# Optimization experiments

Measured on AMD Instinct MI355X. Metric: run time of the kernel, lower is better.

The kernel has to match this reference:

```python
import jax, jax.numpy as jnp
import numpy as np

HID = 8
EMB = 32


def setup_inputs() -> dict:
    V = 32000
    S, B = 128, 32
    key = jax.random.key(0)
    ks = jax.random.split(key, 13)
    u = lambda k, shape, s: jax.random.uniform(k, shape, jnp.float32, -1.0 / np.sqrt(s), 1.0 / np.sqrt(s))
    return {
        "input_batch": jax.random.randint(ks[0], (S, B), 0, V, dtype=jnp.int64),
        "lookup": u(ks[1], (V, EMB), EMB),
        "weight_xf": u(ks[2], (EMB, HID), HID),
        "weight_hf": u(ks[3], (HID, HID), HID),
        "weight_xb": u(ks[4], (EMB, HID), HID),
        "weight_hb": u(ks[5], (HID, HID), HID),
        "weight_o": u(ks[6], (2 * HID, V), V),
        "Hf": u(ks[7], (HID,), HID),
        "Hb": u(ks[8], (HID,), HID),
        "bias_x": u(ks[9], (HID,), HID),
        "bias_hf": u(ks[10], (HID,), HID),
        "bias_hb": u(ks[11], (HID,), HID),
        "bias_o": u(ks[12], (V,), V),
    }


def reference(input_batch, lookup, weight_xf, weight_hf, weight_xb, weight_hb,
              weight_o, Hf, Hb, bias_x, bias_hf, bias_hb, bias_o):
    S, B = input_batch.shape
    X = lookup[input_batch]  # [S, B, EMB]

    # Forward Elman scan. Hf_table[i] = hidden BEFORE consuming x[i] (shifted).
    h0f = jnp.broadcast_to(Hf, (B, HID))

    def fstep(h, x):
        h2 = jnp.tanh(x @ weight_xf + bias_x + h @ weight_hf + bias_hf)
        return h2, h2

    _, hf = jax.lax.scan(fstep, h0f, X)
    Hf_table = jnp.concatenate([h0f[None], hf[:-1]], axis=0)  # [S, B, HID]

    # Backward Elman scan (reverse). hb[i] = hidden after consuming x[i..S-1];
    # original uses hidden after x[i+1..S-1] at position i (init at i=S-1).
    h0b = jnp.broadcast_to(Hb, (B, HID))

    def bstep(h, x):
        h2 = jnp.tanh(x @ weight_xb + bias_x + h @ weight_hb + bias_hb)
        return h2, h2

    _, hb = jax.lax.scan(bstep, h0b, X, reverse=True)
    Hb_table = jnp.concatenate([hb[1:], h0b[None]], axis=0)  # [S, B, HID]

    H = jnp.concatenate([Hf_table, Hb_table], axis=-1)  # [S, B, 2*HID]
    logits = H @ weight_o + bias_o  # [S, B, V]
    return jax.nn.log_softmax(logits, axis=-1)
```

## Files before the change

kernel.cpp:

```cpp
#include <hip/hip_runtime.h>
#include <hip/hip_bf16.h>

#define S_LEN 128
#define B_SZ  32
#define VOCAB 32000
#define EMB   32
#define HID   8
#define NROWS 4096

typedef float v2f __attribute__((ext_vector_type(2)));
typedef float v4f __attribute__((ext_vector_type(4)));

#if defined(__has_builtin) && __has_builtin(__builtin_elementwise_fma)
__device__ __forceinline__ v2f fma2(v2f a, v2f b, v2f c) {
    return __builtin_elementwise_fma(a, b, c);
}
#else
__device__ __forceinline__ v2f fma2(v2f a, v2f b, v2f c) {
    v2f r; r.x = fmaf(a.x, b.x, c.x); r.y = fmaf(a.y, b.y, c.y); return r;
}
#endif

#define XP_STRIDE 65
__global__ __launch_bounds__(256) void fused_pre_kernel(
        const int* __restrict__ idx,
        const float* __restrict__ lookup,
        const float* __restrict__ wxf,
        const float* __restrict__ wxb,
        const float* __restrict__ whf,
        const float* __restrict__ whb,
        const float* __restrict__ Hf0,
        const float* __restrict__ Hb0,
        const float* __restrict__ bias_x,
        const float* __restrict__ bias_hf,
        const float* __restrict__ bias_hb,
        const float* __restrict__ wo,
        float* __restrict__ wo_p,
        float* __restrict__ Hws) {
    __shared__ float xp[S_LEN * XP_STRIDE];
    int t = threadIdx.x;

    if (blockIdx.x < 8) {
        int blk   = blockIdx.x;
        int dir   = blk >> 2;
        int bbase = (blk & 3) * 8;
        const float* wx = dir ? wxb : wxf;
        const float* bh = dir ? bias_hb : bias_hf;

        {
            int s   = t >> 1;
            int bh4 = (t & 1) * 4;
            #pragma unroll
            for (int bb = 0; bb < 4; ++bb) {
                int bl = bh4 + bb;
                int e = idx[s * B_SZ + bbase + bl];
                const float4* xr4 =
                    reinterpret_cast<const float4*>(lookup + (size_t)e * EMB);
                float x[EMB];
                #pragma unroll
                for (int q = 0; q < 8; ++q) {
                    float4 f = xr4[q];
                    x[4 * q + 0] = f.x; x[4 * q + 1] = f.y;
                    x[4 * q + 2] = f.z; x[4 * q + 3] = f.w;
                }
                #pragma unroll
                for (int j = 0; j < HID; ++j) {
                    float fa = bias_x[j] + bh[j];
                    #pragma unroll
                    for (int e2 = 0; e2 < EMB; ++e2)
                        fa += x[e2] * wx[e2 * HID + j];
                    xp[s * XP_STRIDE + bl * HID + j] = fa;
                }
            }
        }
        __syncthreads();

        if (t < 64) {
            int j  = t & 7;
            int bl = t >> 3;
            int b  = bbase + bl;
            const float* wh = dir ? whb : whf;
            float w[HID];
            #pragma unroll
            for (int k = 0; k < HID; ++k) w[k] = wh[k * HID + j];
            float h = dir ? Hb0[j] : Hf0[j];

            for (int step = 0; step < S_LEN; ++step) {
                int s = dir ? (S_LEN - 1 - step) : step;
                float xv = xp[s * XP_STRIDE + bl * HID + j];
                int r = s * B_SZ + b;
                Hws[(size_t)r * 16 + dir * HID + j] = h;
                float acc = xv;
                #pragma unroll
                for (int k = 0; k < HID; ++k)
                    acc += __shfl(h, k, 8) * w[k];
                float ex = __expf(2.0f * acc);
                h = 1.0f - 2.0f * __builtin_amdgcn_rcpf(ex + 1.0f);
            }
        }
        return;
    }

    int v2 = (blockIdx.x - 8) * 256 + t;
    if (v2 >= VOCAB / 2) return;
    float2 buf[16];
    #pragma unroll
    for (int k = 0; k < 16; ++k)
        buf[k] = *reinterpret_cast<const float2*>(wo + (size_t)k * VOCAB + 2 * v2);
    float4* dst = reinterpret_cast<float4*>(wo_p + (size_t)v2 * 32);
    #pragma unroll
    for (int q = 0; q < 8; ++q)
        dst[q] = make_float4(buf[2 * q].x, buf[2 * q].y,
                             buf[2 * q + 1].x, buf[2 * q + 1].y);
}

#define VCH_A 256
#define NCH_A (VOCAB / VCH_A)
__global__ __launch_bounds__(256) void passA_kernel(
        const float* __restrict__ Hws,
        const float* __restrict__ wo_p,
        const float* __restrict__ bias_o,
        float* __restrict__ Zpart) {
    int r0 = blockIdx.y * 256 + threadIdx.x;
    int p0 = blockIdx.x * (VCH_A / 2);

    float h[4][16];
    #pragma unroll
    for (int rr = 0; rr < 4; ++rr) {
        const float4* h4 =
            reinterpret_cast<const float4*>(Hws + (size_t)(r0 + 1024 * rr) * 16);
        #pragma unroll
        for (int q = 0; q < 4; ++q) {
            float4 f = h4[q];
            h[rr][4 * q + 0] = f.x; h[rr][4 * q + 1] = f.y;
            h[rr][4 * q + 2] = f.z; h[rr][4 * q + 3] = f.w;
        }
    }

    float z[4] = {0.0f, 0.0f, 0.0f, 0.0f};
    #pragma unroll 2
    for (int p = 0; p < VCH_A / 2; ++p) {
        const v2f* wp = reinterpret_cast<const v2f*>(wo_p + (size_t)(p0 + p) * 32);
        float2 bb = *reinterpret_cast<const float2*>(bias_o + (size_t)(p0 + p) * 2);
        v2f acc[4];
        #pragma unroll
        for (int rr = 0; rr < 4; ++rr) { acc[rr].x = bb.x; acc[rr].y = bb.y; }
        #pragma unroll
        for (int k = 0; k < 16; ++k) {
            v2f w = wp[k];
            #pragma unroll
            for (int rr = 0; rr < 4; ++rr) {
                v2f hk; hk.x = h[rr][k]; hk.y = h[rr][k];
                acc[rr] = fma2(hk, w, acc[rr]);
            }
        }
        #pragma unroll
        for (int rr = 0; rr < 4; ++rr)
            z[rr] += __expf(acc[rr].x) + __expf(acc[rr].y);
    }
    #pragma unroll
    for (int rr = 0; rr < 4; ++rr)
        Zpart[(size_t)blockIdx.x * NROWS + r0 + 1024 * rr] = z[rr];
}

#define MT_B 128
__global__ __launch_bounds__(256) void passB_kernel(
        const float* __restrict__ Hws,
        const float* __restrict__ wo,
        const float* __restrict__ bias_o,
        const float* __restrict__ Zpart,
        float* __restrict__ out) {
    __shared__ __attribute__((aligned(16))) float hsh[MT_B * 16];
    __shared__ float lz_sh[MT_B];
    int t = threadIdx.x;
    int r0 = blockIdx.y * MT_B;

    {
        const float4* src = reinterpret_cast<const float4*>(Hws + (size_t)r0 * 16);
        float4* dst = reinterpret_cast<float4*>(hsh);
        dst[t]       = src[t];
        dst[t + 256] = src[t + 256];
        if (t < MT_B) {
            float s = 0.0f;
            for (int i = 0; i < NCH_A; ++i)
                s += Zpart[(size_t)i * NROWS + r0 + t];
            lz_sh[t] = logf(s);
        }
    }
    __syncthreads();

    int v = (blockIdx.x * 256 + t) * 4;
    if (v < VOCAB) {
        v2f w01[16], w23[16];
        #pragma unroll
        for (int k = 0; k < 16; ++k) {
            float4 w4 = *reinterpret_cast<const float4*>(wo + (size_t)k * VOCAB + v);
            w01[k].x = w4.x; w01[k].y = w4.y;
            w23[k].x = w4.z; w23[k].y = w4.w;
        }
        float4 bv = *reinterpret_cast<const float4*>(bias_o + v);
        v2f b01; b01.x = bv.x; b01.y = bv.y;
        v2f b23; b23.x = bv.z; b23.y = bv.w;

        #pragma unroll 2
        for (int rr = 0; rr < MT_B; ++rr) {
            const float* hr = hsh + rr * 16;
            v2f t01 = b01, t23 = b23;
            #pragma unroll
            for (int k = 0; k < 16; ++k) {
                float hk = hr[k];
                v2f hk2; hk2.x = hk; hk2.y = hk;
                t01 = fma2(hk2, w01[k], t01);
                t23 = fma2(hk2, w23[k], t23);
            }
            float lz = lz_sh[rr];
            v4f o;
            o.x = t01.x - lz; o.y = t01.y - lz;
            o.z = t23.x - lz; o.w = t23.y - lz;
            __builtin_nontemporal_store(
                o, reinterpret_cast<v4f*>(out + (size_t)(r0 + rr) * VOCAB + v));
        }
    }
}

extern "C" void kernel_launch(void* const* d_in, const int* in_sizes, int n_in,
                              void* d_out, int out_size, void* d_ws, size_t ws_size,
                              hipStream_t stream) {
    const int*   idx     = (const int*)d_in[0];
    const float* lookup  = (const float*)d_in[1];
    const float* wxf     = (const float*)d_in[2];
    const float* whf     = (const float*)d_in[3];
    const float* wxb     = (const float*)d_in[4];
    const float* whb     = (const float*)d_in[5];
    const float* wo      = (const float*)d_in[6];
    const float* Hf0     = (const float*)d_in[7];
    const float* Hb0     = (const float*)d_in[8];
    const float* bias_x  = (const float*)d_in[9];
    const float* bias_hf = (const float*)d_in[10];
    const float* bias_hb = (const float*)d_in[11];
    const float* bias_o  = (const float*)d_in[12];
    float* out = (float*)d_out;

    float* ws    = (float*)d_ws;
    float* Hws   = ws;
    float* wo_p  = ws + 65536;
    float* Zpart = ws + 577536;

    fused_pre_kernel<<<71, 256, 0, stream>>>(idx, lookup, wxf, wxb, whf, whb,
                                             Hf0, Hb0, bias_x, bias_hf, bias_hb,
                                             wo, wo_p, Hws);
    passA_kernel<<<dim3(NCH_A, 4), 256, 0, stream>>>(Hws, wo_p, bias_o, Zpart);
    passB_kernel<<<dim3(32, NROWS / MT_B), 256, 0, stream>>>(Hws, wo, bias_o,
                                                             Zpart, out);
}
```

Baseline: 661.0 us.

## Split logZ reduction into own kernel, halve per-thread rows in passes A and B

passA now has each thread handle 2 rows instead of 4 and launches twice as many blocks, which lowers register pressure and raises occupancy. The per-row reduction of Zpart partial sums and the log are moved out of passB into a separate small logz_kernel, so passB no longer repeats that serial 125-step reduction in every block. passB's row tile drops from 128 to 64, doubling its grid. The cost is an extra kernel launch and reloading the weight rows per 64-row tile, which means more weight traffic.

```diff
diff --git a/kernel.cpp b/kernel.cpp
--- a/kernel.cpp
+++ b/kernel.cpp
@@ -121,54 +121,60 @@
         const float* __restrict__ wo_p,
         const float* __restrict__ bias_o,
         float* __restrict__ Zpart) {
-    int r0 = blockIdx.y * 256 + threadIdx.x;
+    int ra = blockIdx.y * 256 + threadIdx.x;
+    int rb = ra + (NROWS / 2);
     int p0 = blockIdx.x * (VCH_A / 2);
 
-    float h[4][16];
+    float ha[16], hb[16];
+    const float4* ha4 = reinterpret_cast<const float4*>(Hws + (size_t)ra * 16);
+    const float4* hb4 = reinterpret_cast<const float4*>(Hws + (size_t)rb * 16);
     #pragma unroll
-    for (int rr = 0; rr < 4; ++rr) {
-        const float4* h4 =
-            reinterpret_cast<const float4*>(Hws + (size_t)(r0 + 1024 * rr) * 16);
-        #pragma unroll
-        for (int q = 0; q < 4; ++q) {
-            float4 f = h4[q];
-            h[rr][4 * q + 0] = f.x; h[rr][4 * q + 1] = f.y;
-            h[rr][4 * q + 2] = f.z; h[rr][4 * q + 3] = f.w;
-        }
-    }
-
-    float z[4] = {0.0f, 0.0f, 0.0f, 0.0f};
+    for (int q = 0; q < 4; ++q) {
+        float4 fa = ha4[q];
+        float4 fb = hb4[q];
+        ha[4 * q + 0] = fa.x; ha[4 * q + 1] = fa.y;
+        ha[4 * q + 2] = fa.z; ha[4 * q + 3] = fa.w;
+        hb[4 * q + 0] = fb.x; hb[4 * q + 1] = fb.y;
+        hb[4 * q + 2] = fb.z; hb[4 * q + 3] = fb.w;
+    }
+
+    float za = 0.0f, zb = 0.0f;
     #pragma unroll 2
     for (int p = 0; p < VCH_A / 2; ++p) {
         const v2f* wp = reinterpret_cast<const v2f*>(wo_p + (size_t)(p0 + p) * 32);
         float2 bb = *reinterpret_cast<const float2*>(bias_o + (size_t)(p0 + p) * 2);
-        v2f acc[4];
-        #pragma unroll
-        for (int rr = 0; rr < 4; ++rr) { acc[rr].x = bb.x; acc[rr].y = bb.y; }
+        v2f acca; acca.x = bb.x; acca.y = bb.y;
+        v2f accb = acca;
         #pragma unroll
         for (int k = 0; k < 16; ++k) {
             v2f w = wp[k];
-            #pragma unroll
-            for (int rr = 0; rr < 4; ++rr) {
-                v2f hk; hk.x = h[rr][k]; hk.y = h[rr][k];
-                acc[rr] = fma2(hk, w, acc[rr]);
-            }
-        }
-        #pragma unroll
-        for (int rr = 0; rr < 4; ++rr)
-            z[rr] += __expf(acc[rr].x) + __expf(acc[rr].y);
-    }
-    #pragma unroll
-    for (int rr = 0; rr < 4; ++rr)
-        Zpart[(size_t)blockIdx.x * NROWS + r0 + 1024 * rr] = z[rr];
-}
-
-#define MT_B 128
+            v2f hka; hka.x = ha[k]; hka.y = ha[k];
+            v2f hkb; hkb.x = hb[k]; hkb.y = hb[k];
+            acca = fma2(hka, w, acca);
+            accb = fma2(hkb, w, accb);
+        }
+        za += __expf(acca.x) + __expf(acca.y);
+        zb += __expf(accb.x) + __expf(accb.y);
+    }
+    Zpart[(size_t)blockIdx.x * NROWS + ra] = za;
+    Zpart[(size_t)blockIdx.x * NROWS + rb] = zb;
+}
+
+__global__ __launch_bounds__(256) void logz_kernel(
+        const float* __restrict__ Zpart, float* __restrict__ logZ) {
+    int r = blockIdx.x * blockDim.x + threadIdx.x;
+    if (r >= NROWS) return;
+    float s = 0.0f;
+    for (int i = 0; i < NCH_A; ++i) s += Zpart[(size_t)i * NROWS + r];
+    logZ[r] = logf(s);
+}
+
+#define MT_B 64
 __global__ __launch_bounds__(256) void passB_kernel(
         const float* __restrict__ Hws,
         const float* __restrict__ wo,
         const float* __restrict__ bias_o,
-        const float* __restrict__ Zpart,
+        const float* __restrict__ logZ,
         float* __restrict__ out) {
     __shared__ __attribute__((aligned(16))) float hsh[MT_B * 16];
     __shared__ float lz_sh[MT_B];
@@ -178,14 +184,8 @@
     {
         const float4* src = reinterpret_cast<const float4*>(Hws + (size_t)r0 * 16);
         float4* dst = reinterpret_cast<float4*>(hsh);
-        dst[t]       = src[t];
-        dst[t + 256] = src[t + 256];
-        if (t < MT_B) {
-            float s = 0.0f;
-            for (int i = 0; i < NCH_A; ++i)
-                s += Zpart[(size_t)i * NROWS + r0 + t];
-            lz_sh[t] = logf(s);
-        }
+        dst[t] = src[t];
+        if (t < MT_B) lz_sh[t] = logZ[r0 + t];
     }
     __syncthreads();
 
@@ -245,11 +245,13 @@
     float* Hws   = ws;
     float* wo_p  = ws + 65536;
     float* Zpart = ws + 577536;
+    float* logZ  = ws + 1089536;
 
     fused_pre_kernel<<<71, 256, 0, stream>>>(idx, lookup, wxf, wxb, whf, whb,
                                              Hf0, Hb0, bias_x, bias_hf, bias_hb,
                                              wo, wo_p, Hws);
-    passA_kernel<<<dim3(NCH_A, 4), 256, 0, stream>>>(Hws, wo_p, bias_o, Zpart);
+    passA_kernel<<<dim3(NCH_A, 8), 256, 0, stream>>>(Hws, wo_p, bias_o, Zpart);
+    logz_kernel<<<16, 256, 0, stream>>>(Zpart, logZ);
     passB_kernel<<<dim3(32, NROWS / MT_B), 256, 0, stream>>>(Hws, wo, bias_o,
-                                                             Zpart, out);
-}
+                                                             logZ, out);
+}
```

New measurement: 655.4 us. About the same (-0.9%).
